# Kernel tuning notes

Measured on AMD Instinct MI355X. Metric: run time of the kernel, lower is better.

## Reference

```python
import jax, jax.numpy as jnp
import numpy as np

N_G, E_G = 50000, 800000
N_S, E_S = 10000, 160000
NF = 64
B = 8

def _w(key, shape):
    fan_in = shape[-1]
    return jax.random.normal(key, shape, dtype=jnp.float32) / np.sqrt(fan_in)

def setup_inputs() -> dict:
    key = jax.random.key(0)
    ks = jax.random.split(key, 40)
    inp = {
        "graph_x": jax.random.normal(ks[0], (N_G, NF), dtype=jnp.float32),
        "subgraph_x": jax.random.normal(ks[1], (N_S, NF), dtype=jnp.float32),
        "point": jax.random.normal(ks[2], (B, NF), dtype=jnp.float32),
        "graph_edge_index": jax.random.randint(ks[3], (2, E_G), 0, N_G),
        "graph_batch": jnp.sort(jax.random.randint(ks[4], (N_G,), 0, B)),
        "subgraph_edge_index": jax.random.randint(ks[5], (2, E_S), 0, N_S),
        "subgraph_batch": jnp.sort(jax.random.randint(ks[6], (N_S,), 0, B)),
    }
    # GraphConv params per branch: channel sizes 64->128->256->192
    dims = [(2 * NF, NF), (4 * NF, 2 * NF), (3 * NF, 4 * NF)]
    i = 7
    for pre in ("g", "s"):
        for li, (o, c) in enumerate(dims, start=1):
            inp[f"{pre}W{li}r"] = _w(ks[i], (o, c)); i += 1  # lin_rel (aggregated)
            inp[f"{pre}W{li}n"] = _w(ks[i], (o, c)); i += 1  # lin_root (self)
            inp[f"{pre}B{li}"] = jnp.zeros((o,), dtype=jnp.float32)
    inp["l1W"] = _w(ks[i], (600, 3 * NF + 3 * NF + NF)); i += 1
    inp["l1b"] = jnp.zeros((600,), dtype=jnp.float32)
    inp["l2W"] = _w(ks[i], (256, 600)); i += 1
    inp["l2b"] = jnp.zeros((256,), dtype=jnp.float32)
    inp["l3W"] = _w(ks[i], (NF, 256)); i += 1
    inp["l3b"] = jnp.zeros((NF,), dtype=jnp.float32)
    return inp

def _graph_conv(x, src, dst, Wr, Wn, b, n_nodes):
    # PyG GraphConv: out_i = Wr @ sum_{j->i} x_j + Wn @ x_i + b
    agg = jax.ops.segment_sum(x[src], dst, num_segments=n_nodes)
    return agg @ Wr.T + x @ Wn.T + b

def _scatter_mean(x, seg, num_segments):
    s = jax.ops.segment_sum(x, seg, num_segments=num_segments)
    cnt = jax.ops.segment_sum(jnp.ones((x.shape[0],), x.dtype), seg, num_segments=num_segments)
    return s / jnp.maximum(cnt, 1.0)[:, None]

def _branch(x, edge_index, batch, params, n_nodes):
    src, dst = edge_index[0], edge_index[1]
    for (Wr, Wn, b) in params:
        x = jax.nn.elu(_graph_conv(x, src, dst, Wr, Wn, b, n_nodes))
    return _scatter_mean(x, batch, B)

def reference(graph_x, subgraph_x, point,
              gW1r, gW1n, gB1, gW2r, gW2n, gB2, gW3r, gW3n, gB3,
              sW1r, sW1n, sB1, sW2r, sW2n, sB2, sW3r, sW3n, sB3,
              l1W, l1b, l2W, l2b, l3W, l3b,
              graph_edge_index, graph_batch, subgraph_edge_index, subgraph_batch):
    x1 = _branch(graph_x, graph_edge_index, graph_batch,
                 [(gW1r, gW1n, gB1), (gW2r, gW2n, gB2), (gW3r, gW3n, gB3)], N_G)
    x2 = _branch(subgraph_x, subgraph_edge_index, subgraph_batch,
                 [(sW1r, sW1n, sB1), (sW2r, sW2n, sB2), (sW3r, sW3n, sB3)], N_S)
    x = jnp.concatenate([x1, x2, point], axis=-1)  # [B, 448]
    x = jax.nn.relu(x @ l1W.T + l1b)
    x = jax.nn.relu(x @ l2W.T + l2b)
    return x @ l3W.T + l3b  # [B, 64]
```

## Files before the change

### kernel.cpp

```cpp
#include <hip/hip_runtime.h>
#include <cmath>

typedef __attribute__((ext_vector_type(8))) short short8;
typedef __attribute__((ext_vector_type(4))) short shortx4;
typedef __attribute__((ext_vector_type(4))) float floatx4;
typedef __attribute__((ext_vector_type(2))) float floatx2;
typedef __attribute__((ext_vector_type(4))) int intx4;
typedef __attribute__((ext_vector_type(2))) int intx2;

#define N_G 50000
#define E_G 800000
#define N_S 10000
#define E_S 160000
#define NT (N_G + N_S)
#define ET (E_G + E_S)
#define BATCH 8
#define STRIDE 64
#define FPASS 8

__device__ __forceinline__ float b2f(short s) {
    unsigned u = ((unsigned)(unsigned short)s) << 16;
    return __builtin_bit_cast(float, u);
}
__device__ __forceinline__ short f2b(float f) {
    unsigned u = __builtin_bit_cast(unsigned, f);
    u += 0x7FFF + ((u >> 16) & 1);
    return (short)(u >> 16);
}
__device__ __forceinline__ short8 fp8x8_to_bf16(intx2 w) {
    floatx2 f0 = __builtin_amdgcn_cvt_pk_f32_fp8(w[0], false);
    floatx2 f1 = __builtin_amdgcn_cvt_pk_f32_fp8(w[0], true);
    floatx2 f2 = __builtin_amdgcn_cvt_pk_f32_fp8(w[1], false);
    floatx2 f3 = __builtin_amdgcn_cvt_pk_f32_fp8(w[1], true);
    short8 r;
    r[0]=f2b(f0[0]); r[1]=f2b(f0[1]); r[2]=f2b(f1[0]); r[3]=f2b(f1[1]);
    r[4]=f2b(f2[0]); r[5]=f2b(f2[1]); r[6]=f2b(f3[0]); r[7]=f2b(f3[1]);
    return r;
}

struct RepArgs { const float* Wr[6]; const float* Wn[6]; short* dst[6]; int cin[6]; int nk[6]; int groups[6]; };
__global__ void init_kernel(const float* __restrict__ gx, const float* __restrict__ sx,
                            unsigned char* __restrict__ X0_8,
                            int* __restrict__ dcount, float* __restrict__ pooled,
                            const int* __restrict__ g_batch, const int* __restrict__ s_batch,
                            int* __restrict__ starts, RepArgs ra, int total_groups) {
    int t = blockIdx.x * blockDim.x + threadIdx.x;
    if (t < NT * 16) {
        size_t e = (size_t)t * 4;
        const float* src = (e < (size_t)N_G * 64) ? (gx + e) : (sx + (e - (size_t)N_G * 64));
        floatx4 v = *(const floatx4*)src;
        int w8 = 0;
        w8 = __builtin_amdgcn_cvt_pk_fp8_f32(v[0], v[1], w8, false);
        w8 = __builtin_amdgcn_cvt_pk_fp8_f32(v[2], v[3], w8, true);
        *(unsigned int*)(X0_8 + e) = (unsigned int)w8;
    }
    if (t < NT) dcount[t] = 0;
    if (t < 16 * 192) pooled[t] = 0.f;
    if (t <= 16) {
        int b = t;
        if (b == 16) { starts[16] = NT; }
        else {
            int key, n, base;
            const int* arr;
            if (b < 8) { arr = g_batch; n = N_G; key = b; base = 0; }
            else       { arr = s_batch; n = N_S; key = b - 8; base = N_G; }
            int lo = 0, hi = n;
            while (lo < hi) { int mid = (lo + hi) >> 1; if (arr[mid] < key) lo = mid + 1; else hi = mid; }
            starts[b] = base + lo;
        }
    }
    if (t < total_groups) {
        int seg = 0, off = t;
        while (seg < 5 && off >= ra.groups[seg]) { off -= ra.groups[seg]; ++seg; }
        int CIN = ra.cin[seg], NK = ra.nk[seg];
        int lane = off & 63;
        int rest = off >> 6;
        int tt = rest % NK;
        int ot = rest / NK;
        int o = ot * 16 + (lane & 15);
        int kk = tt * 32 + (lane >> 4) * 8;
        const float* src = (kk < CIN) ? (ra.Wr[seg] + (size_t)o * CIN + kk)
                                      : (ra.Wn[seg] + (size_t)o * CIN + (kk - CIN));
        floatx4 u0 = *(const floatx4*)src;
        floatx4 u1 = *(const floatx4*)(src + 4);
        short8 d;
        d[0]=f2b(u0[0]); d[1]=f2b(u0[1]); d[2]=f2b(u0[2]); d[3]=f2b(u0[3]);
        d[4]=f2b(u1[0]); d[5]=f2b(u1[1]); d[6]=f2b(u1[2]); d[7]=f2b(u1[3]);
        *(short8*)(ra.dst[seg] + (size_t)off * 8) = d;
    }
}

__global__ void fill_kernel(const int* __restrict__ g_ei, const int* __restrict__ s_ei,
                            int* __restrict__ dcount, int* __restrict__ csr) {
    int pass = blockIdx.x & (FPASS - 1);
    int lb   = blockIdx.x >> 3;
    int t = lb * blockDim.x + threadIdx.x;
    if (t >= ET) return;
    int dst;
    if (t < E_G) dst = g_ei[E_G + t];
    else         dst = s_ei[E_S + (t - E_G)] + N_G;
    int lo = pass * (NT / FPASS);
    int hi = lo + (NT / FPASS);
    if (dst < lo || dst >= hi) return;
    int src;
    if (t < E_G) src = g_ei[t];
    else         src = s_ei[t - E_G] + N_G;
    int slot = atomicAdd(&dcount[dst], 1);
    if (slot < STRIDE) csr[(size_t)dst * STRIDE + slot] = src;
}

template<int C>
__global__ void agg8_kernel(const unsigned char* __restrict__ x8, const int* __restrict__ dcount,
                            const int* __restrict__ csr, short* __restrict__ out) {
    constexpr int C16 = C / 16;
    int t = blockIdx.x * blockDim.x + threadIdx.x;
    if (t >= NT * C16) return;
    int node = t / C16;
    int ch   = t % C16;
    int e0 = node * STRIDE;
    int e1 = e0 + min(dcount[node], STRIDE);
    float acc[16];
    #pragma unroll
    for (int j = 0; j < 16; ++j) acc[j] = 0.f;
    for (int e = e0; e < e1; ++e) {
        int s = csr[e];
        intx4 w = *(const intx4*)(x8 + (size_t)s * C + ch * 16);
        #pragma unroll
        for (int q = 0; q < 4; ++q) {
            floatx2 f0 = __builtin_amdgcn_cvt_pk_f32_fp8(w[q], false);
            floatx2 f1 = __builtin_amdgcn_cvt_pk_f32_fp8(w[q], true);
            acc[q * 4 + 0] += f0[0];
            acc[q * 4 + 1] += f0[1];
            acc[q * 4 + 2] += f1[0];
            acc[q * 4 + 3] += f1[1];
        }
    }
    short8 o0, o1;
    #pragma unroll
    for (int j = 0; j < 8; ++j) { o0[j] = f2b(acc[j]); o1[j] = f2b(acc[8 + j]); }
    short8* q = (short8*)(out + (size_t)node * C + ch * 16);
    q[0] = o0; q[1] = o1;
}

template<int CIN, int COUT, bool POOL>
__global__ __launch_bounds__(256) void gemm_elu_kernel(
        const short* __restrict__ A1, const unsigned char* __restrict__ A2_8,
        const short* __restrict__ gWF, const short* __restrict__ sWF,
        const float* __restrict__ gB, const float* __restrict__ sB,
        unsigned char* __restrict__ out8,
        float* __restrict__ pooled, const int* __restrict__ starts) {
    constexpr int NK  = CIN / 16;
    constexpr int NOT = COUT / 16;
    int wave = (blockIdx.x * blockDim.x + threadIdx.x) >> 6;
    int lane = threadIdx.x & 63;
    int r0 = wave * 16;
    if (r0 >= NT) return;
    bool sub = (r0 >= N_G);
    const short* WF = sub ? sWF : gWF;
    const float* bias = sub ? sB : gB;
    int id = lane & 15, quad = lane >> 4;
    int arow = r0 + id;
    short8 a[NK];
    #pragma unroll
    for (int t = 0; t < NK; ++t) {
        int kk = t * 32 + quad * 8;
        if (kk < CIN) {
            a[t] = *(const short8*)(A1 + (size_t)arow * CIN + kk);
        } else {
            intx2 w = *(const intx2*)(A2_8 + (size_t)arow * CIN + (kk - CIN));
            a[t] = fp8x8_to_bf16(w);
        }
    }
    int seg0 = 0, seg1 = 0;
    if (POOL) {
        while (seg0 < 15 && starts[seg0 + 1] <= r0) ++seg0;
        seg1 = seg0;
        while (seg1 < 15 && starts[seg1 + 1] <= r0 + 15) ++seg1;
    }
    for (int ot = 0; ot < NOT; ++ot) {
        floatx4 acc = {0.f, 0.f, 0.f, 0.f};
        const short* wp = WF + (((size_t)ot * NK) * 64 + lane) * 8;
        #pragma unroll
        for (int t = 0; t < NK; ++t) {
            short8 b = *(const short8*)(wp + (size_t)t * 64 * 8);
            acc = __builtin_amdgcn_mfma_f32_16x16x32_bf16(a[t], b, acc, 0, 0, 0);
        }
        int o = ot * 16 + id;
        float bv = bias[o];
        float vr[4];
        #pragma unroll
        for (int r = 0; r < 4; ++r) {
            float v = acc[r] + bv;
            vr[r] = (v > 0.f) ? v : (expf(v) - 1.f);
        }
        if (!POOL) {
            #pragma unroll
            for (int r = 0; r < 4; ++r) {
                int nrow = r0 + quad * 4 + r;
                int w8 = __builtin_amdgcn_cvt_pk_fp8_f32(vr[r], vr[r], 0, false);
                out8[(size_t)nrow * COUT + o] = (unsigned char)(w8 & 0xFF);
            }
        } else if (seg0 == seg1) {
            float vsum = vr[0] + vr[1] + vr[2] + vr[3];
            vsum += __shfl_down(vsum, 32, 64);
            vsum += __shfl_down(vsum, 16, 64);
            if (lane < 16) atomicAdd(&pooled[seg0 * 192 + o], vsum);
        } else {
            #pragma unroll
            for (int r = 0; r < 4; ++r) {
                int nrow = r0 + quad * 4 + r;
                int sg = seg0;
                while (sg < seg1 && starts[sg + 1] <= nrow) ++sg;
                atomicAdd(&pooled[sg * 192 + o], vr[r]);
            }
        }
    }
}

__global__ __launch_bounds__(256) void mlp1_kernel(
        const float* __restrict__ pooled, const int* __restrict__ starts,
        const float* __restrict__ point, const float* __restrict__ W,
        const float* __restrict__ bias, float* __restrict__ out) {
    int wave = (blockIdx.x * blockDim.x + threadIdx.x) >> 6;
    int lane = threadIdx.x & 63;
    if (wave >= BATCH * 600) return;
    int b = wave / 600, o = wave % 600;
    float invg = 1.f / (float)max(starts[b + 1] - starts[b], 1);
    float invs = 1.f / (float)max(starts[9 + b] - starts[8 + b], 1);
    const float* w = W + (size_t)o * 448;
    float acc = 0.f;
    for (int i = lane; i < 448; i += 64) {
        float x;
        if (i < 192)      x = pooled[b * 192 + i] * invg;
        else if (i < 384) x = pooled[(8 + b) * 192 + (i - 192)] * invs;
        else              x = point[b * 64 + (i - 384)];
        acc += x * w[i];
    }
    #pragma unroll
    for (int off = 32; off > 0; off >>= 1) acc += __shfl_down(acc, off, 64);
    if (lane == 0) out[wave] = fmaxf(acc + bias[o], 0.f);
}

__global__ __launch_bounds__(256) void dense_wave_kernel(
        const float* __restrict__ in, const float* __restrict__ W,
        const float* __restrict__ bias, float* __restrict__ out,
        int I, int O, int relu) {
    int wave = (blockIdx.x * blockDim.x + threadIdx.x) >> 6;
    int lane = threadIdx.x & 63;
    if (wave >= BATCH * O) return;
    int b = wave / O, o = wave % O;
    const float* x = in + (size_t)b * I;
    const float* w = W + (size_t)o * I;
    float acc = 0.f;
    for (int i = lane; i < I; i += 64) acc += x[i] * w[i];
    #pragma unroll
    for (int off = 32; off > 0; off >>= 1) acc += __shfl_down(acc, off, 64);
    if (lane == 0) {
        acc += bias[o];
        if (relu) acc = fmaxf(acc, 0.f);
        out[wave] = acc;
    }
}

extern "C" void kernel_launch(void* const* d_in, const int* in_sizes, int n_in,
                              void* d_out, int out_size, void* d_ws, size_t ws_size,
                              hipStream_t stream) {
    const float* graph_x = (const float*)d_in[0];
    const float* sub_x   = (const float*)d_in[1];
    const float* point   = (const float*)d_in[2];
    const int*   g_ei    = (const int*)d_in[3];
    const int*   g_batch = (const int*)d_in[4];
    const int*   s_ei    = (const int*)d_in[5];
    const int*   s_batch = (const int*)d_in[6];
    const float* gB1=(const float*)d_in[9],  *gB2=(const float*)d_in[12], *gB3=(const float*)d_in[15];
    const float* sB1=(const float*)d_in[18], *sB2=(const float*)d_in[21], *sB3=(const float*)d_in[24];
    const float* l1W=(const float*)d_in[25], *l1b=(const float*)d_in[26];
    const float* l2W=(const float*)d_in[27], *l2b=(const float*)d_in[28];
    const float* l3W=(const float*)d_in[29], *l3b=(const float*)d_in[30];

    char* ws = (char*)d_ws;
    size_t off = 0;
    auto alloc = [&](size_t bytes) -> char* {
        char* p = ws + off;
        off = (off + bytes + 255) & ~(size_t)255;
        return p;
    };
    int* dcount = (int*)alloc((size_t)NT * 4);
    int* csr = (int*)alloc((size_t)NT * STRIDE * 4);

    const int fsz[3] = {128 * 2 * 64, 256 * 2 * 128, 192 * 2 * 256};
    short* wfrag = (short*)alloc((size_t)(fsz[0] + fsz[1] + fsz[2]) * 2 * 2);
    short* gWF[3], *sWF[3];
    { size_t o2 = 0;
      for (int l = 0; l < 3; ++l) { gWF[l] = wfrag + o2; o2 += fsz[l]; }
      for (int l = 0; l < 3; ++l) { sWF[l] = wfrag + o2; o2 += fsz[l]; } }

    unsigned char* X0_8 = (unsigned char*)alloc((size_t)NT * 64);
    short* agg = (short*)alloc((size_t)NT * 256 * 2);
    unsigned char* h1_8 = (unsigned char*)alloc((size_t)NT * 128);
    unsigned char* h2_8 = (unsigned char*)alloc((size_t)NT * 256);

    float* pooled = (float*)alloc(16 * 192 * 4);
    int* starts = (int*)alloc(17 * 4);
    float* mlp_h1 = (float*)alloc(BATCH * 600 * 4);
    float* mlp_h2 = (float*)alloc(BATCH * 256 * 4);

    RepArgs ra;
    const int cin_l[3] = {64, 128, 256};
    const int nk_l[3]  = {4, 8, 16};
    const int not_l[3] = {8, 16, 12};
    const int wr_idx[6] = {7, 10, 13, 16, 19, 22};
    int total_groups = 0;
    for (int s = 0; s < 6; ++s) {
        int l = s % 3;
        ra.Wr[s] = (const float*)d_in[wr_idx[s]];
        ra.Wn[s] = (const float*)d_in[wr_idx[s] + 1];
        ra.dst[s] = (s < 3) ? gWF[l] : sWF[l];
        ra.cin[s] = cin_l[l];
        ra.nk[s] = nk_l[l];
        ra.groups[s] = not_l[l] * nk_l[l] * 64;
        total_groups += ra.groups[s];
    }

    init_kernel<<<(NT * 16 + 255) / 256, 256, 0, stream>>>(graph_x, sub_x, X0_8, dcount,
                                                           pooled, g_batch, s_batch, starts,
                                                           ra, total_groups);

    fill_kernel<<<((ET + 255) / 256) * FPASS, 256, 0, stream>>>(g_ei, s_ei, dcount, csr);

    constexpr int NW = NT / 16;
    const int gemm_blocks = (NW + 3) / 4;

    agg8_kernel<64><<<(NT * 4 + 255) / 256, 256, 0, stream>>>(X0_8, dcount, csr, agg);
    gemm_elu_kernel<64, 128, false><<<gemm_blocks, 256, 0, stream>>>(
        agg, X0_8, gWF[0], sWF[0], gB1, sB1, h1_8, nullptr, nullptr);
    agg8_kernel<128><<<(NT * 8 + 255) / 256, 256, 0, stream>>>(h1_8, dcount, csr, agg);
    gemm_elu_kernel<128, 256, false><<<gemm_blocks, 256, 0, stream>>>(
        agg, h1_8, gWF[1], sWF[1], gB2, sB2, h2_8, nullptr, nullptr);
    agg8_kernel<256><<<(NT * 16 + 255) / 256, 256, 0, stream>>>(h2_8, dcount, csr, agg);
    gemm_elu_kernel<256, 192, true><<<gemm_blocks, 256, 0, stream>>>(
        agg, h2_8, gWF[2], sWF[2], gB3, sB3, nullptr, pooled, starts);

    mlp1_kernel<<<(BATCH * 600 + 3) / 4, 256, 0, stream>>>(pooled, starts, point, l1W, l1b, mlp_h1);
    dense_wave_kernel<<<(BATCH * 256 + 3) / 4, 256, 0, stream>>>(mlp_h1, l2W, l2b, mlp_h2, 600, 256, 1);
    dense_wave_kernel<<<(BATCH * 64 + 3) / 4, 256, 0, stream>>>(mlp_h2, l3W, l3b, (float*)d_out, 256, 64, 0);
}
```

Before: 378.5 us.

## Stage GraphConv weight slices in LDS and tile GEMM over output slices

The fused GraphConv GEMM+ELU kernel is restructured so each block loads one output-channel slice of the packed bf16 weights into shared memory using global_load_lds. Blocks are split by graph or subgraph and by weight slice, and each wave processes one or two 16-row tiles against that slice. The aim is to stop re-reading the weights from global memory for every 16-row tile and to reuse B fragments across several row tiles. The trade-off is that A rows are now re-read once per output slice, there is extra LDS pressure, and grid sizes are hard-coded. It also switches expf to __expf.

```diff
diff --git a/kernel.cpp b/kernel.cpp
--- a/kernel.cpp
+++ b/kernel.cpp
@@ -2,7 +2,6 @@
 #include <cmath>
 
 typedef __attribute__((ext_vector_type(8))) short short8;
-typedef __attribute__((ext_vector_type(4))) short shortx4;
 typedef __attribute__((ext_vector_type(4))) float floatx4;
 typedef __attribute__((ext_vector_type(2))) float floatx2;
 typedef __attribute__((ext_vector_type(4))) int intx4;
@@ -18,10 +17,6 @@
 #define STRIDE 64
 #define FPASS 8
 
-__device__ __forceinline__ float b2f(short s) {
-    unsigned u = ((unsigned)(unsigned short)s) << 16;
-    return __builtin_bit_cast(float, u);
-}
 __device__ __forceinline__ short f2b(float f) {
     unsigned u = __builtin_bit_cast(unsigned, f);
     u += 0x7FFF + ((u >> 16) & 1);
@@ -36,6 +31,11 @@
     r[0]=f2b(f0[0]); r[1]=f2b(f0[1]); r[2]=f2b(f1[0]); r[3]=f2b(f1[1]);
     r[4]=f2b(f2[0]); r[5]=f2b(f2[1]); r[6]=f2b(f3[0]); r[7]=f2b(f3[1]);
     return r;
+}
+__device__ __forceinline__ void gload_lds16(const void* g, void* l) {
+    __builtin_amdgcn_global_load_lds(
+        (const __attribute__((address_space(1))) unsigned int*)g,
+        (__attribute__((address_space(3))) unsigned int*)l, 16, 0, 0);
 }
 
 struct RepArgs { const float* Wr[6]; const float* Wn[6]; short* dst[6]; int cin[6]; int nk[6]; int groups[6]; };
@@ -142,76 +142,130 @@
     q[0] = o0; q[1] = o1;
 }
 
-template<int CIN, int COUT, bool POOL>
+template<int CIN, int COUT, int OT, int MROW, bool POOL>
 __global__ __launch_bounds__(256) void gemm_elu_kernel(
         const short* __restrict__ A1, const unsigned char* __restrict__ A2_8,
         const short* __restrict__ gWF, const short* __restrict__ sWF,
         const float* __restrict__ gB, const float* __restrict__ sB,
         unsigned char* __restrict__ out8,
-        float* __restrict__ pooled, const int* __restrict__ starts) {
+        float* __restrict__ pooled, const int* __restrict__ starts,
+        int RGg, int RGs) {
     constexpr int NK  = CIN / 16;
-    constexpr int NOT = COUT / 16;
-    int wave = (blockIdx.x * blockDim.x + threadIdx.x) >> 6;
+    constexpr int TILE_SH = NK * 512;
+    constexpr int CH_SH = OT * TILE_SH;
+    constexpr int SREG = CH_SH / 2048;
+    constexpr int KH   = (NK > 8) ? 2 : 1;
+    constexpr int NKH  = NK / KH;
+    constexpr int TG = N_G / 16, TS = (NT - N_G) / 16;
+    __shared__ short lds[CH_SH];
+
+    int RB = RGg + RGs;
+    int slice = blockIdx.x / RB;
+    int r = blockIdx.x - slice * RB;
+    bool isg = (r < RGg);
+    int rpart = isg ? r : (r - RGg);
+    int baseT = isg ? 0 : TG;
+    int Tpart = isg ? TG : TS;
+    int Wpart = (isg ? RGg : RGs) * 4;
+    const short* WF = (isg ? gWF : sWF) + (size_t)slice * CH_SH;
+    const float* bias = isg ? gB : sB;
+
+    {
+        const short* src = WF + threadIdx.x * 8;
+        short* dst = &lds[threadIdx.x * 8];
+        #pragma unroll
+        for (int i = 0; i < SREG; ++i)
+            gload_lds16(src + i * 2048, dst + i * 2048);
+    }
+    __syncthreads();
+
+    int wave = threadIdx.x >> 6;
     int lane = threadIdx.x & 63;
-    int r0 = wave * 16;
-    if (r0 >= NT) return;
-    bool sub = (r0 >= N_G);
-    const short* WF = sub ? sWF : gWF;
-    const float* bias = sub ? sB : gB;
     int id = lane & 15, quad = lane >> 4;
-    int arow = r0 + id;
-    short8 a[NK];
-    #pragma unroll
-    for (int t = 0; t < NK; ++t) {
-        int kk = t * 32 + quad * 8;
-        if (kk < CIN) {
-            a[t] = *(const short8*)(A1 + (size_t)arow * CIN + kk);
-        } else {
-            intx2 w = *(const intx2*)(A2_8 + (size_t)arow * CIN + (kk - CIN));
-            a[t] = fp8x8_to_bf16(w);
-        }
-    }
-    int seg0 = 0, seg1 = 0;
-    if (POOL) {
-        while (seg0 < 15 && starts[seg0 + 1] <= r0) ++seg0;
-        seg1 = seg0;
-        while (seg1 < 15 && starts[seg1 + 1] <= r0 + 15) ++seg1;
-    }
-    for (int ot = 0; ot < NOT; ++ot) {
-        floatx4 acc = {0.f, 0.f, 0.f, 0.f};
-        const short* wp = WF + (((size_t)ot * NK) * 64 + lane) * 8;
-        #pragma unroll
-        for (int t = 0; t < NK; ++t) {
-            short8 b = *(const short8*)(wp + (size_t)t * 64 * 8);
-            acc = __builtin_amdgcn_mfma_f32_16x16x32_bf16(a[t], b, acc, 0, 0, 0);
-        }
-        int o = ot * 16 + id;
-        float bv = bias[o];
-        float vr[4];
-        #pragma unroll
-        for (int r = 0; r < 4; ++r) {
-            float v = acc[r] + bv;
-            vr[r] = (v > 0.f) ? v : (expf(v) - 1.f);
-        }
-        if (!POOL) {
+    int units = (Tpart + MROW - 1) / MROW;
+
+    for (int u = rpart * 4 + wave; u < units; u += Wpart) {
+        int tl[MROW]; bool act[MROW];
+        #pragma unroll
+        for (int m = 0; m < MROW; ++m) {
+            int ti = u * MROW + m;
+            act[m] = (ti < Tpart);
+            tl[m] = baseT + (act[m] ? ti : (Tpart - 1));
+        }
+        floatx4 acc[MROW][OT];
+        #pragma unroll
+        for (int m = 0; m < MROW; ++m)
             #pragma unroll
-            for (int r = 0; r < 4; ++r) {
-                int nrow = r0 + quad * 4 + r;
-                int w8 = __builtin_amdgcn_cvt_pk_fp8_f32(vr[r], vr[r], 0, false);
-                out8[(size_t)nrow * COUT + o] = (unsigned char)(w8 & 0xFF);
+            for (int o = 0; o < OT; ++o) acc[m][o] = floatx4{0.f, 0.f, 0.f, 0.f};
+
+        for (int kh = 0; kh < KH; ++kh) {
+            short8 a[MROW][NKH];
+            #pragma unroll
+            for (int m = 0; m < MROW; ++m) {
+                int arow = tl[m] * 16 + id;
+                #pragma unroll
+                for (int t = 0; t < NKH; ++t) {
+                    int kk = (kh * NKH + t) * 32 + quad * 8;
+                    if (kk < CIN) {
+                        a[m][t] = *(const short8*)(A1 + (size_t)arow * CIN + kk);
+                    } else {
+                        intx2 w = *(const intx2*)(A2_8 + (size_t)arow * CIN + (kk - CIN));
+                        a[m][t] = fp8x8_to_bf16(w);
+                    }
+                }
             }
-        } else if (seg0 == seg1) {
-            float vsum = vr[0] + vr[1] + vr[2] + vr[3];
-            vsum += __shfl_down(vsum, 32, 64);
-            vsum += __shfl_down(vsum, 16, 64);
-            if (lane < 16) atomicAdd(&pooled[seg0 * 192 + o], vsum);
-        } else {
             #pragma unroll
-            for (int r = 0; r < 4; ++r) {
-                int nrow = r0 + quad * 4 + r;
-                int sg = seg0;
-                while (sg < seg1 && starts[sg + 1] <= nrow) ++sg;
-                atomicAdd(&pooled[sg * 192 + o], vr[r]);
+            for (int otl = 0; otl < OT; ++otl) {
+                #pragma unroll
+                for (int t = 0; t < NKH; ++t) {
+                    short8 b = *(const short8*)(&lds[((size_t)otl * NK + kh * NKH + t) * 512 + lane * 8]);
+                    #pragma unroll
+                    for (int m = 0; m < MROW; ++m)
+                        acc[m][otl] = __builtin_amdgcn_mfma_f32_16x16x32_bf16(a[m][t], b, acc[m][otl], 0, 0, 0);
+                }
+            }
+        }
+        #pragma unroll
+        for (int m = 0; m < MROW; ++m) {
+            if (!act[m]) continue;
+            int r0 = tl[m] * 16;
+            int seg0 = 0, seg1 = 0;
+            if (POOL) {
+                while (seg0 < 15 && starts[seg0 + 1] <= r0) ++seg0;
+                seg1 = seg0;
+                while (seg1 < 15 && starts[seg1 + 1] <= r0 + 15) ++seg1;
+            }
+            #pragma unroll
+            for (int otl = 0; otl < OT; ++otl) {
+                int o = (slice * OT + otl) * 16 + id;
+                float bv = bias[o];
+                float vr[4];
+                #pragma unroll
+                for (int rr = 0; rr < 4; ++rr) {
+                    float v = acc[m][otl][rr] + bv;
+                    vr[rr] = (v > 0.f) ? v : (__expf(v) - 1.f);
+                }
+                if (!POOL) {
+                    #pragma unroll
+                    for (int rr = 0; rr < 4; ++rr) {
+                        int nrow = r0 + quad * 4 + rr;
+                        int w8 = __builtin_amdgcn_cvt_pk_fp8_f32(vr[rr], vr[rr], 0, false);
+                        out8[(size_t)nrow * COUT + o] = (unsigned char)(w8 & 0xFF);
+                    }
+                } else if (seg0 == seg1) {
+                    float vsum = vr[0] + vr[1] + vr[2] + vr[3];
+                    vsum += __shfl_down(vsum, 32, 64);
+                    vsum += __shfl_down(vsum, 16, 64);
+                    if (lane < 16) atomicAdd(&pooled[seg0 * 192 + o], vsum);
+                } else {
+                    #pragma unroll
+                    for (int rr = 0; rr < 4; ++rr) {
+                        int nrow = r0 + quad * 4 + rr;
+                        int sg = seg0;
+                        while (sg < seg1 && starts[sg + 1] <= nrow) ++sg;
+                        atomicAdd(&pooled[sg * 192 + o], vr[rr]);
+                    }
+                }
             }
         }
     }
@@ -328,18 +382,15 @@
 
     fill_kernel<<<((ET + 255) / 256) * FPASS, 256, 0, stream>>>(g_ei, s_ei, dcount, csr);
 
-    constexpr int NW = NT / 16;
-    const int gemm_blocks = (NW + 3) / 4;
-
     agg8_kernel<64><<<(NT * 4 + 255) / 256, 256, 0, stream>>>(X0_8, dcount, csr, agg);
-    gemm_elu_kernel<64, 128, false><<<gemm_blocks, 256, 0, stream>>>(
-        agg, X0_8, gWF[0], sWF[0], gB1, sB1, h1_8, nullptr, nullptr);
+    gemm_elu_kernel<64, 128, 8, 1, false><<<939, 256, 0, stream>>>(
+        agg, X0_8, gWF[0], sWF[0], gB1, sB1, h1_8, nullptr, nullptr, 782, 157);
     agg8_kernel<128><<<(NT * 8 + 255) / 256, 256, 0, stream>>>(h1_8, dcount, csr, agg);
-    gemm_elu_kernel<128, 256, false><<<gemm_blocks, 256, 0, stream>>>(
-        agg, h1_8, gWF[1], sWF[1], gB2, sB2, h2_8, nullptr, nullptr);
+    gemm_elu_kernel<128, 256, 4, 2, false><<<1880, 256, 0, stream>>>(
+        agg, h1_8, gWF[1], sWF[1], gB2, sB2, h2_8, nullptr, nullptr, 391, 79);
     agg8_kernel<256><<<(NT * 16 + 255) / 256, 256, 0, stream>>>(h2_8, dcount, csr, agg);
-    gemm_elu_kernel<256, 192, true><<<gemm_blocks, 256, 0, stream>>>(
-        agg, h2_8, gWF[2], sWF[2], gB3, sB3, nullptr, pooled, starts);
+    gemm_elu_kernel<256, 192, 2, 2, true><<<2820, 256, 0, stream>>>(
+        agg, h2_8, gWF[2], sWF[2], gB3, sB3, nullptr, pooled, starts, 391, 79);
 
     mlp1_kernel<<<(BATCH * 600 + 3) / 4, 256, 0, stream>>>(pooled, starts, point, l1W, l1b, mlp_h1);
     dense_wave_kernel<<<(BATCH * 256 + 3) / 4, 256, 0, stream>>>(mlp_h1, l2W, l2b, mlp_h2, 600, 256, 1);
```

Result: slower. 398.0 us (+5.1%).

## Split GEMM-ELU output columns across blocks with K-halving and fast exp

Applied to the files above, without the earlier changes.

Rewrites the per-layer GEMM+ELU kernel so each block of two waves handles two row tiles and one slice of the output channels. The slice index is interleaved with the row-group index in the block id, and large K is processed in two halves to cut register pressure. Launch bounds change to 128 threads with 5 blocks per SM, and expf is replaced by __expf. This is meant to raise parallelism and occupancy instead of having one wave loop over all output tiles. The cost is that the A rows are reloaded once per column slice.

```diff
diff --git a/kernel.cpp b/kernel.cpp
--- a/kernel.cpp
+++ b/kernel.cpp
@@ -2,7 +2,6 @@
 #include <cmath>
 
 typedef __attribute__((ext_vector_type(8))) short short8;
-typedef __attribute__((ext_vector_type(4))) short shortx4;
 typedef __attribute__((ext_vector_type(4))) float floatx4;
 typedef __attribute__((ext_vector_type(2))) float floatx2;
 typedef __attribute__((ext_vector_type(4))) int intx4;
@@ -18,10 +17,6 @@
 #define STRIDE 64
 #define FPASS 8
 
-__device__ __forceinline__ float b2f(short s) {
-    unsigned u = ((unsigned)(unsigned short)s) << 16;
-    return __builtin_bit_cast(float, u);
-}
 __device__ __forceinline__ short f2b(float f) {
     unsigned u = __builtin_bit_cast(unsigned, f);
     u += 0x7FFF + ((u >> 16) & 1);
@@ -142,8 +137,8 @@
     q[0] = o0; q[1] = o1;
 }
 
-template<int CIN, int COUT, bool POOL>
-__global__ __launch_bounds__(256) void gemm_elu_kernel(
+template<int CIN, int COUT, int C, bool POOL>
+__global__ __launch_bounds__(128, 5) void gemm_elu_kernel(
         const short* __restrict__ A1, const unsigned char* __restrict__ A2_8,
         const short* __restrict__ gWF, const short* __restrict__ sWF,
         const float* __restrict__ gB, const float* __restrict__ sB,
@@ -151,53 +146,79 @@
         float* __restrict__ pooled, const int* __restrict__ starts) {
     constexpr int NK  = CIN / 16;
     constexpr int NOT = COUT / 16;
-    int wave = (blockIdx.x * blockDim.x + threadIdx.x) >> 6;
+    constexpr int OTW = NOT / C;
+    static_assert(NOT % C == 0, "C must divide NOT");
+    constexpr int KH  = (NK > 8) ? 2 : 1;
+    constexpr int NKH = NK / KH;
+    constexpr int NTILE = NT / 16;
+    constexpr int RG = NTILE / 2;
+    constexpr int TSUB = N_G / 16;
+
+    int rg8 = blockIdx.x & 7;
+    int rest = blockIdx.x >> 3;
+    int c = rest % C;
+    int rg = (rest / C) * 8 + rg8;
+    if (rg >= RG) return;
+
+    int wid = threadIdx.x >> 6;
     int lane = threadIdx.x & 63;
-    int r0 = wave * 16;
-    if (r0 >= NT) return;
-    bool sub = (r0 >= N_G);
-    const short* WF = sub ? sWF : gWF;
+    int id = lane & 15, quad = lane >> 4;
+    int tile = rg * 2 + wid;
+    bool sub = (tile >= TSUB);
+    const short* WFl = sub ? sWF : gWF;
     const float* bias = sub ? sB : gB;
-    int id = lane & 15, quad = lane >> 4;
+    int r0 = tile * 16;
     int arow = r0 + id;
-    short8 a[NK];
-    #pragma unroll
-    for (int t = 0; t < NK; ++t) {
-        int kk = t * 32 + quad * 8;
-        if (kk < CIN) {
-            a[t] = *(const short8*)(A1 + (size_t)arow * CIN + kk);
-        } else {
-            intx2 w = *(const intx2*)(A2_8 + (size_t)arow * CIN + (kk - CIN));
-            a[t] = fp8x8_to_bf16(w);
-        }
-    }
+
     int seg0 = 0, seg1 = 0;
     if (POOL) {
         while (seg0 < 15 && starts[seg0 + 1] <= r0) ++seg0;
         seg1 = seg0;
         while (seg1 < 15 && starts[seg1 + 1] <= r0 + 15) ++seg1;
     }
-    for (int ot = 0; ot < NOT; ++ot) {
-        floatx4 acc = {0.f, 0.f, 0.f, 0.f};
-        const short* wp = WF + (((size_t)ot * NK) * 64 + lane) * 8;
+
+    floatx4 acc[OTW];
+    #pragma unroll
+    for (int o = 0; o < OTW; ++o) acc[o] = floatx4{0.f, 0.f, 0.f, 0.f};
+
+    for (int kh = 0; kh < KH; ++kh) {
+        short8 a[NKH];
         #pragma unroll
-        for (int t = 0; t < NK; ++t) {
-            short8 b = *(const short8*)(wp + (size_t)t * 64 * 8);
-            acc = __builtin_amdgcn_mfma_f32_16x16x32_bf16(a[t], b, acc, 0, 0, 0);
-        }
-        int o = ot * 16 + id;
+        for (int t = 0; t < NKH; ++t) {
+            int kk = (kh * NKH + t) * 32 + quad * 8;
+            if (kk < CIN) {
+                a[t] = *(const short8*)(A1 + (size_t)arow * CIN + kk);
+            } else {
+                intx2 w = *(const intx2*)(A2_8 + (size_t)arow * CIN + (kk - CIN));
+                a[t] = fp8x8_to_bf16(w);
+            }
+        }
+        #pragma unroll
+        for (int otl = 0; otl < OTW; ++otl) {
+            const short* wp = WFl + ((((size_t)(c * OTW + otl) * NK + kh * NKH) * 64) + lane) * 8;
+            #pragma unroll
+            for (int t = 0; t < NKH; ++t) {
+                short8 b = *(const short8*)(wp + (size_t)t * 512);
+                acc[otl] = __builtin_amdgcn_mfma_f32_16x16x32_bf16(a[t], b, acc[otl], 0, 0, 0);
+            }
+        }
+    }
+
+    #pragma unroll
+    for (int otl = 0; otl < OTW; ++otl) {
+        int o = (c * OTW + otl) * 16 + id;
         float bv = bias[o];
         float vr[4];
         #pragma unroll
-        for (int r = 0; r < 4; ++r) {
-            float v = acc[r] + bv;
-            vr[r] = (v > 0.f) ? v : (expf(v) - 1.f);
+        for (int rr = 0; rr < 4; ++rr) {
+            float v = acc[otl][rr] + bv;
+            vr[rr] = (v > 0.f) ? v : (__expf(v) - 1.f);
         }
         if (!POOL) {
             #pragma unroll
-            for (int r = 0; r < 4; ++r) {
-                int nrow = r0 + quad * 4 + r;
-                int w8 = __builtin_amdgcn_cvt_pk_fp8_f32(vr[r], vr[r], 0, false);
+            for (int rr = 0; rr < 4; ++rr) {
+                int nrow = r0 + quad * 4 + rr;
+                int w8 = __builtin_amdgcn_cvt_pk_fp8_f32(vr[rr], vr[rr], 0, false);
                 out8[(size_t)nrow * COUT + o] = (unsigned char)(w8 & 0xFF);
             }
         } else if (seg0 == seg1) {
@@ -207,11 +228,11 @@
             if (lane < 16) atomicAdd(&pooled[seg0 * 192 + o], vsum);
         } else {
             #pragma unroll
-            for (int r = 0; r < 4; ++r) {
-                int nrow = r0 + quad * 4 + r;
+            for (int rr = 0; rr < 4; ++rr) {
+                int nrow = r0 + quad * 4 + rr;
                 int sg = seg0;
                 while (sg < seg1 && starts[sg + 1] <= nrow) ++sg;
-                atomicAdd(&pooled[sg * 192 + o], vr[r]);
+                atomicAdd(&pooled[sg * 192 + o], vr[rr]);
             }
         }
     }
@@ -328,17 +349,14 @@
 
     fill_kernel<<<((ET + 255) / 256) * FPASS, 256, 0, stream>>>(g_ei, s_ei, dcount, csr);
 
-    constexpr int NW = NT / 16;
-    const int gemm_blocks = (NW + 3) / 4;
-
     agg8_kernel<64><<<(NT * 4 + 255) / 256, 256, 0, stream>>>(X0_8, dcount, csr, agg);
-    gemm_elu_kernel<64, 128, false><<<gemm_blocks, 256, 0, stream>>>(
+    gemm_elu_kernel<64, 128, 2, false><<<235 * 2 * 8, 128, 0, stream>>>(
         agg, X0_8, gWF[0], sWF[0], gB1, sB1, h1_8, nullptr, nullptr);
     agg8_kernel<128><<<(NT * 8 + 255) / 256, 256, 0, stream>>>(h1_8, dcount, csr, agg);
-    gemm_elu_kernel<128, 256, false><<<gemm_blocks, 256, 0, stream>>>(
+    gemm_elu_kernel<128, 256, 4, false><<<235 * 4 * 8, 128, 0, stream>>>(
         agg, h1_8, gWF[1], sWF[1], gB2, sB2, h2_8, nullptr, nullptr);
     agg8_kernel<256><<<(NT * 16 + 255) / 256, 256, 0, stream>>>(h2_8, dcount, csr, agg);
-    gemm_elu_kernel<256, 192, true><<<gemm_blocks, 256, 0, stream>>>(
+    gemm_elu_kernel<256, 192, 4, true><<<235 * 4 * 8, 128, 0, stream>>>(
         agg, h2_8, gWF[2], sWF[2], gB3, sB3, nullptr, pooled, starts);
 
     mlp1_kernel<<<(BATCH * 600 + 3) / 4, 256, 0, stream>>>(pooled, starts, point, l1W, l1b, mlp_h1);
```

After: 393.2 us. +3.9%, slower.
